# Kernel tuning notes

Hardware: AMD Instinct MI355X
Metric: run time of the kernel (lower is better)

The kernel has to match this reference:

```python
import jax, jax.numpy as jnp
import numpy as np


def fake_quant(w, bits):
    # Symmetric per-tensor fake quantization with straight-through estimator.
    qmax = 2.0 ** (bits - 1) - 1.0
    scale = jnp.max(jnp.abs(w)) / qmax
    wq = jnp.clip(jnp.round(w / scale), -qmax, qmax) * scale
    return w + jax.lax.stop_gradient(wq - w)


def setup_inputs() -> dict:
    key = jax.random.key(0)
    k = jax.random.split(key, 5)
    B, S, D, H = 64, 196, 768, 3072
    x = jax.random.normal(k[0], (B, S, D), dtype=jnp.float32)
    w1 = jax.random.normal(k[1], (H, D), dtype=jnp.float32) * (1.0 / np.sqrt(D))
    b1 = jax.random.normal(k[2], (H,), dtype=jnp.float32) * 0.01
    w2 = jax.random.normal(k[3], (D, H), dtype=jnp.float32) * (1.0 / np.sqrt(H))
    b2 = jax.random.normal(k[4], (D,), dtype=jnp.float32) * 0.01
    return {"x": x, "w1": w1, "b1": b1, "w2": w2, "b2": b2, "bits": 8}


def reference(x, w1, b1, w2, b2, bits):
    # fc1 (fake-quant weight) -> ReLU -> fc2 (fake-quant weight)
    w1q = fake_quant(w1, bits)
    w2q = fake_quant(w2, bits)
    h = jnp.einsum('bsd,hd->bsh', x, w1q) + b1   # [B,S,3072]
    h = jax.nn.relu(h)
    out = jnp.einsum('bsh,dh->bsd', h, w2q) + b2  # [B,S,768]
    return out
```

## Files before the change

### kernel.cpp

```cpp
#include <hip/hip_runtime.h>
#include <hip/hip_bf16.h>
#include <stdint.h>

typedef __attribute__((ext_vector_type(8))) short bf16x8;
typedef __attribute__((ext_vector_type(4))) float f32x4;

__device__ __forceinline__ unsigned short f2bf(float f) {
  __hip_bfloat16 h = __float2bfloat16(f);
  return *reinterpret_cast<unsigned short*>(&h);
}

__global__ void prep_kernel(const float* __restrict__ w1, const float* __restrict__ w2,
                            const float* __restrict__ x, int n4w, int n4x,
                            unsigned int* __restrict__ out_scales,
                            unsigned short* __restrict__ ox) {
  if (blockIdx.y == 2) {
    const float4* x4 = reinterpret_cast<const float4*>(x);
    ushort4* o4 = reinterpret_cast<ushort4*>(ox);
    for (int i = blockIdx.x * blockDim.x + threadIdx.x; i < n4x;
         i += gridDim.x * blockDim.x) {
      float4 v = x4[i];
      o4[i] = make_ushort4(f2bf(v.x), f2bf(v.y), f2bf(v.z), f2bf(v.w));
    }
    return;
  }
  const float* w = blockIdx.y ? w2 : w1;
  __shared__ unsigned int red[256];
  unsigned int m = 0u;
  const uint4* w4 = reinterpret_cast<const uint4*>(w);
  for (int i = blockIdx.x * blockDim.x + threadIdx.x; i < n4w;
       i += gridDim.x * blockDim.x) {
    uint4 v = w4[i];
    m = max(m, v.x & 0x7fffffffu);
    m = max(m, v.y & 0x7fffffffu);
    m = max(m, v.z & 0x7fffffffu);
    m = max(m, v.w & 0x7fffffffu);
  }
  red[threadIdx.x] = m;
  __syncthreads();
  for (int s = 128; s > 0; s >>= 1) {
    if ((int)threadIdx.x < s)
      red[threadIdx.x] = max(red[threadIdx.x], red[threadIdx.x + s]);
    __syncthreads();
  }
  if (threadIdx.x == 0) atomicMax(out_scales + blockIdx.y, red[0]);
}

__global__ void quant2_kernel(const float* __restrict__ w1, const float* __restrict__ w2,
                              int n4, const unsigned int* __restrict__ maxbits,
                              const int* __restrict__ bits,
                              unsigned short* __restrict__ o1, unsigned short* __restrict__ o2) {
  const float* w = blockIdx.y ? w2 : w1;
  unsigned short* o = blockIdx.y ? o2 : o1;
  const float qmax = (float)((1 << (*bits - 1)) - 1);
  const float scale = __uint_as_float(maxbits[blockIdx.y]) / qmax;
  const float4* w4 = reinterpret_cast<const float4*>(w);
  ushort4* o4 = reinterpret_cast<ushort4*>(o);
  for (int i = blockIdx.x * blockDim.x + threadIdx.x; i < n4;
       i += gridDim.x * blockDim.x) {
    float4 v = w4[i];
    float a = fminf(fmaxf(rintf(v.x / scale), -qmax), qmax) * scale;
    float b = fminf(fmaxf(rintf(v.y / scale), -qmax), qmax) * scale;
    float c = fminf(fmaxf(rintf(v.z / scale), -qmax), qmax) * scale;
    float d = fminf(fmaxf(rintf(v.w / scale), -qmax), qmax) * scale;
    o4[i] = make_ushort4(f2bf(a), f2bf(b), f2bf(c), f2bf(d));
  }
}

template<int BM, bool PRIO, bool RELU, bool BF16_OUT>
__global__ __launch_bounds__(256)
void gemm_bt(const unsigned short* __restrict__ A,
             const unsigned short* __restrict__ B,
             const float* __restrict__ bias,
             void* __restrict__ Cout,
             int M, int N, int K, int gx) {
  constexpr int BK = 64;
  constexpr int MF = BM / 32;
  __shared__ __attribute__((aligned(16))) unsigned short As[2][BM * BK];
  __shared__ __attribute__((aligned(16))) unsigned short Bs[2][128 * BK];

  const int nwg = gridDim.x;
  const int orig = blockIdx.x;
  const int q = nwg >> 3, r = nwg & 7;
  const int xcd = orig & 7, cidx = orig >> 3;
  const int wgid = (xcd < r ? xcd * (q + 1) : r * (q + 1) + (xcd - r) * q) + cidx;
  const int bx = wgid % gx;
  const int by = wgid / gx;

  const int tid = threadIdx.x;
  const int lane = tid & 63;
  const int wave = tid >> 6;
  const int wr = wave >> 1;
  const int wc = wave & 1;
  const long brow = (long)by * BM;
  const long bcol = (long)bx * 128;

  f32x4 acc[MF][4] = {};

  const int srow = lane >> 3;
  const int gslot = ((lane & 7) ^ (lane >> 3)) * 8;
  const int fr = lane & 15;
  const int fs = lane >> 4;

  auto stage = [&](int k0, int b) {
#pragma unroll
    for (int it = 0; it < BM / 32; ++it) {
      const int c = it * 4 + wave;
      const unsigned short* ga = A + (brow + c * 8 + srow) * (long)K + k0 + gslot;
      __builtin_amdgcn_global_load_lds(
          (const __attribute__((address_space(1))) void*)ga,
          (__attribute__((address_space(3))) void*)(&As[b][c * 512]), 16, 0, 0);
    }
#pragma unroll
    for (int it = 0; it < 4; ++it) {
      const int c = it * 4 + wave;
      const unsigned short* gb = B + (bcol + c * 8 + srow) * (long)K + k0 + gslot;
      __builtin_amdgcn_global_load_lds(
          (const __attribute__((address_space(1))) void*)gb,
          (__attribute__((address_space(3))) void*)(&Bs[b][c * 512]), 16, 0, 0);
    }
  };

  const int nt = K / BK;
  stage(0, 0);
  stage(BK, 1);

  for (int t = 0; t < nt; ++t) {
    const int b = t & 1;
    if (t < nt - 1) {
      if constexpr (BM == 128) asm volatile("s_waitcnt vmcnt(8)" ::: "memory");
      else                     asm volatile("s_waitcnt vmcnt(6)" ::: "memory");
    } else {
      asm volatile("s_waitcnt vmcnt(0)" ::: "memory");
    }
    __builtin_amdgcn_s_barrier();

    const unsigned short* as = &As[b][0];
    const unsigned short* bs = &Bs[b][0];
#pragma unroll
    for (int kk = 0; kk < 2; ++kk) {
      const int s = kk * 4 + fs;
      bf16x8 a[MF], bb[4];
#pragma unroll
      for (int m = 0; m < MF; ++m) {
        const int row = wr * (MF * 16) + m * 16 + fr;
        a[m] = *reinterpret_cast<const bf16x8*>(as + row * BK + ((s ^ (row & 7)) * 8));
      }
#pragma unroll
      for (int n = 0; n < 4; ++n) {
        const int row = wc * 64 + n * 16 + fr;
        bb[n] = *reinterpret_cast<const bf16x8*>(bs + row * BK + ((s ^ (row & 7)) * 8));
      }
      if (PRIO) __builtin_amdgcn_s_setprio(1);
#pragma unroll
      for (int m = 0; m < MF; ++m)
#pragma unroll
        for (int n = 0; n < 4; ++n)
          acc[m][n] = __builtin_amdgcn_mfma_f32_16x16x32_bf16(a[m], bb[n], acc[m][n], 0, 0, 0);
      if (PRIO) __builtin_amdgcn_s_setprio(0);
    }

    asm volatile("s_waitcnt lgkmcnt(0)" ::: "memory");
    __builtin_amdgcn_sched_barrier(0);
    __builtin_amdgcn_s_barrier();
    if (t + 2 < nt) stage((t + 2) * BK, b);
  }

  const int fq = lane >> 4;
#pragma unroll
  for (int n = 0; n < 4; ++n) {
    const long col = bcol + wc * 64 + n * 16 + fr;
    const float bv = bias[col];
#pragma unroll
    for (int m = 0; m < MF; ++m) {
#pragma unroll
      for (int rr = 0; rr < 4; ++rr) {
        const long row = brow + wr * (MF * 16) + m * 16 + fq * 4 + rr;
        float v = acc[m][n][rr] + bv;
        if (RELU) v = fmaxf(v, 0.0f);
        if (BF16_OUT)
          ((unsigned short*)Cout)[row * N + col] = f2bf(v);
        else
          ((float*)Cout)[row * N + col] = v;
      }
    }
  }
}

extern "C" void kernel_launch(void* const* d_in, const int* in_sizes, int n_in,
                              void* d_out, int out_size, void* d_ws, size_t ws_size,
                              hipStream_t stream) {
  const float* x  = (const float*)d_in[0];
  const float* w1 = (const float*)d_in[1];
  const float* b1 = (const float*)d_in[2];
  const float* w2 = (const float*)d_in[3];
  const float* b2 = (const float*)d_in[4];
  const int* bits = (const int*)d_in[5];

  const int M = 64 * 196;
  const int D = 768, H = 3072;
  const int nx = M * D;
  const int nw1 = H * D;

  char* ws = (char*)d_ws;
  unsigned int* scales = (unsigned int*)ws;
  unsigned short* xb  = (unsigned short*)(ws + 256);
  unsigned short* w1q = (unsigned short*)(ws + 256 + (size_t)nx * 2);
  unsigned short* w2q = (unsigned short*)(ws + 256 + (size_t)nx * 2 + (size_t)nw1 * 2);
  unsigned short* hb  = (unsigned short*)(ws + 256 + (size_t)nx * 2 + (size_t)nw1 * 4);

  hipMemsetAsync(scales, 0, 8, stream);
  prep_kernel<<<dim3(512, 3), 256, 0, stream>>>(w1, w2, x, nw1 / 4, nx / 4, scales, xb);
  quant2_kernel<<<dim3(512, 2), 256, 0, stream>>>(w1, w2, nw1 / 4, scales, bits, w1q, w2q);

  gemm_bt<128, false, true, true><<<(H / 128) * (M / 128), 256, 0, stream>>>(
      xb, w1q, b1, hb, M, H, D, H / 128);
  gemm_bt<64, true, false, false><<<(D / 128) * (M / 64), 256, 0, stream>>>(
      hb, w2q, b2, d_out, M, D, H, D / 128);
}
```

Measured before the change: 194.3 us.

## Use BK=32 GEMM for fc1 and replace atomic max with two-stage reduction

fc1 now runs on a new GEMM kernel with a 32-wide K tile. That halves LDS per block, and with launch bounds of 3 it aims for more resident workgroups per CU to hide latency. The swizzle pattern is adjusted for the narrower rows. The weight abs-max is now reduced through per-block partials, stored temporarily in the hidden buffer, then finished inside the quant kernel. This removes the memset and the atomics. In exchange, each fc1 K-step gets more barrier overhead, and each quant block re-reduces 512 partials.

```diff
diff --git a/kernel.cpp b/kernel.cpp
--- a/kernel.cpp
+++ b/kernel.cpp
@@ -12,7 +12,7 @@
 
 __global__ void prep_kernel(const float* __restrict__ w1, const float* __restrict__ w2,
                             const float* __restrict__ x, int n4w, int n4x,
-                            unsigned int* __restrict__ out_scales,
+                            unsigned int* __restrict__ pmax,
                             unsigned short* __restrict__ ox) {
   if (blockIdx.y == 2) {
     const float4* x4 = reinterpret_cast<const float4*>(x);
@@ -43,17 +43,27 @@
       red[threadIdx.x] = max(red[threadIdx.x], red[threadIdx.x + s]);
     __syncthreads();
   }
-  if (threadIdx.x == 0) atomicMax(out_scales + blockIdx.y, red[0]);
+  if (threadIdx.x == 0) pmax[blockIdx.y * 512 + blockIdx.x] = red[0];
 }
 
 __global__ void quant2_kernel(const float* __restrict__ w1, const float* __restrict__ w2,
-                              int n4, const unsigned int* __restrict__ maxbits,
+                              int n4, const unsigned int* __restrict__ pmax,
                               const int* __restrict__ bits,
                               unsigned short* __restrict__ o1, unsigned short* __restrict__ o2) {
+  __shared__ unsigned int red[256];
+  const unsigned int* p = pmax + blockIdx.y * 512;
+  red[threadIdx.x] = max(p[threadIdx.x], p[threadIdx.x + 256]);
+  __syncthreads();
+  for (int s = 128; s > 0; s >>= 1) {
+    if ((int)threadIdx.x < s)
+      red[threadIdx.x] = max(red[threadIdx.x], red[threadIdx.x + s]);
+    __syncthreads();
+  }
+  const float qmax = (float)((1 << (*bits - 1)) - 1);
+  const float scale = __uint_as_float(red[0]) / qmax;
+
   const float* w = blockIdx.y ? w2 : w1;
   unsigned short* o = blockIdx.y ? o2 : o1;
-  const float qmax = (float)((1 << (*bits - 1)) - 1);
-  const float scale = __uint_as_float(maxbits[blockIdx.y]) / qmax;
   const float4* w4 = reinterpret_cast<const float4*>(w);
   ushort4* o4 = reinterpret_cast<ushort4*>(o);
   for (int i = blockIdx.x * blockDim.x + threadIdx.x; i < n4;
@@ -67,12 +77,119 @@
   }
 }
 
+template<bool RELU, bool BF16_OUT>
+__global__ __launch_bounds__(256, 3)
+void gemm_bt32(const unsigned short* __restrict__ A,
+               const unsigned short* __restrict__ B,
+               const float* __restrict__ bias,
+               void* __restrict__ Cout,
+               int M, int N, int K, int gx) {
+  constexpr int BK = 32, MF = 4;
+  __shared__ __attribute__((aligned(16))) unsigned short As[2][128 * BK];
+  __shared__ __attribute__((aligned(16))) unsigned short Bs[2][128 * BK];
+
+  const int nwg = gridDim.x;
+  const int orig = blockIdx.x;
+  const int q = nwg >> 3, r = nwg & 7;
+  const int xcd = orig & 7, cidx = orig >> 3;
+  const int wgid = (xcd < r ? xcd * (q + 1) : r * (q + 1) + (xcd - r) * q) + cidx;
+  const int bx = wgid % gx;
+  const int by = wgid / gx;
+
+  const int tid = threadIdx.x;
+  const int lane = tid & 63;
+  const int wave = tid >> 6;
+  const int wr = wave >> 1;
+  const int wc = wave & 1;
+  const long brow = (long)by * 128;
+  const long bcol = (long)bx * 128;
+
+  f32x4 acc[MF][4] = {};
+
+  const int srow = lane >> 2;
+  const int gslot = ((lane & 3) ^ ((lane >> 3) & 3)) * 8;
+  const int fr = lane & 15;
+  const int fs = lane >> 4;
+
+  auto stage = [&](int k0, int b) {
+#pragma unroll
+    for (int it = 0; it < 2; ++it) {
+      const int c = it * 4 + wave;
+      const unsigned short* ga = A + (brow + c * 16 + srow) * (long)K + k0 + gslot;
+      __builtin_amdgcn_global_load_lds(
+          (const __attribute__((address_space(1))) void*)ga,
+          (__attribute__((address_space(3))) void*)(&As[b][c * 512]), 16, 0, 0);
+    }
+#pragma unroll
+    for (int it = 0; it < 2; ++it) {
+      const int c = it * 4 + wave;
+      const unsigned short* gb = B + (bcol + c * 16 + srow) * (long)K + k0 + gslot;
+      __builtin_amdgcn_global_load_lds(
+          (const __attribute__((address_space(1))) void*)gb,
+          (__attribute__((address_space(3))) void*)(&Bs[b][c * 512]), 16, 0, 0);
+    }
+  };
+
+  const int nt = K / BK;
+  stage(0, 0);
+  stage(BK, 1);
+
+  for (int t = 0; t < nt; ++t) {
+    const int b = t & 1;
+    if (t < nt - 1) asm volatile("s_waitcnt vmcnt(4)" ::: "memory");
+    else            asm volatile("s_waitcnt vmcnt(0)" ::: "memory");
+    __builtin_amdgcn_s_barrier();
+
+    const unsigned short* as = &As[b][0];
+    const unsigned short* bs = &Bs[b][0];
+    bf16x8 a[MF], bb[4];
+#pragma unroll
+    for (int m = 0; m < MF; ++m) {
+      const int row = wr * 64 + m * 16 + fr;
+      a[m] = *reinterpret_cast<const bf16x8*>(as + row * BK + ((fs ^ ((row >> 1) & 3)) * 8));
+    }
+#pragma unroll
+    for (int n = 0; n < 4; ++n) {
+      const int row = wc * 64 + n * 16 + fr;
+      bb[n] = *reinterpret_cast<const bf16x8*>(bs + row * BK + ((fs ^ ((row >> 1) & 3)) * 8));
+    }
+#pragma unroll
+    for (int m = 0; m < MF; ++m)
+#pragma unroll
+      for (int n = 0; n < 4; ++n)
+        acc[m][n] = __builtin_amdgcn_mfma_f32_16x16x32_bf16(a[m], bb[n], acc[m][n], 0, 0, 0);
+
+    asm volatile("s_waitcnt lgkmcnt(0)" ::: "memory");
+    __builtin_amdgcn_sched_barrier(0);
+    __builtin_amdgcn_s_barrier();
+    if (t + 2 < nt) stage((t + 2) * BK, b);
+  }
+
+  const int fq = lane >> 4;
+#pragma unroll
+  for (int n = 0; n < 4; ++n) {
+    const long col = bcol + wc * 64 + n * 16 + fr;
+    const float bv = bias[col];
+#pragma unroll
+    for (int m = 0; m < MF; ++m) {
+#pragma unroll
+      for (int rr = 0; rr < 4; ++rr) {
+        const long row = brow + wr * 64 + m * 16 + fq * 4 + rr;
+        float v = acc[m][n][rr] + bv;
+        if (RELU) v = fmaxf(v, 0.0f);
+        if (BF16_OUT)
+          ((unsigned short*)Cout)[row * N + col] = f2bf(v);
+        else
+          ((float*)Cout)[row * N + col] = v;
+      }
+    }
+  }
+}
+
 template<int BM, bool PRIO, bool RELU, bool BF16_OUT>
 __global__ __launch_bounds__(256)
-void gemm_bt(const unsigned short* __restrict__ A,
-             const unsigned short* __restrict__ B,
-             const float* __restrict__ bias,
-             void* __restrict__ Cout,
+void gemm_bt(const unsigned short* __restrict__ A, const unsigned short* __restrict__ B,
+             const float* __restrict__ bias, void* __restrict__ Cout,
              int M, int N, int K, int gx) {
   constexpr int BK = 64;
   constexpr int MF = BM / 32;
@@ -203,17 +320,16 @@
   const int nw1 = H * D;
 
   char* ws = (char*)d_ws;
-  unsigned int* scales = (unsigned int*)ws;
   unsigned short* xb  = (unsigned short*)(ws + 256);
   unsigned short* w1q = (unsigned short*)(ws + 256 + (size_t)nx * 2);
   unsigned short* w2q = (unsigned short*)(ws + 256 + (size_t)nx * 2 + (size_t)nw1 * 2);
   unsigned short* hb  = (unsigned short*)(ws + 256 + (size_t)nx * 2 + (size_t)nw1 * 4);
-
-  hipMemsetAsync(scales, 0, 8, stream);
-  prep_kernel<<<dim3(512, 3), 256, 0, stream>>>(w1, w2, x, nw1 / 4, nx / 4, scales, xb);
-  quant2_kernel<<<dim3(512, 2), 256, 0, stream>>>(w1, w2, nw1 / 4, scales, bits, w1q, w2q);
-
-  gemm_bt<128, false, true, true><<<(H / 128) * (M / 128), 256, 0, stream>>>(
+  unsigned int* pmax = (unsigned int*)hb;
+
+  prep_kernel<<<dim3(512, 3), 256, 0, stream>>>(w1, w2, x, nw1 / 4, nx / 4, pmax, xb);
+  quant2_kernel<<<dim3(512, 2), 256, 0, stream>>>(w1, w2, nw1 / 4, pmax, bits, w1q, w2q);
+
+  gemm_bt32<true, true><<<(H / 128) * (M / 128), 256, 0, stream>>>(
       xb, w1q, b1, hb, M, H, D, H / 128);
   gemm_bt<64, true, false, false><<<(D / 128) * (M / 64), 256, 0, stream>>>(
       hb, w2q, b2, d_out, M, D, H, D / 128);
```

Measured after the change: 184.4 us. -5.1%, faster.
